# Optimization experiments

Hardware: AMD Instinct MI355X
Metric: run time of the kernel (lower is better)

Reference implementation:

```python
import jax, jax.numpy as jnp
import numpy as np
from jax import lax

B = 4096        # batch
D = 13          # state dim (13th component is constant context)
STEPS = 16      # output time points
SUBSTEPS = 2    # fixed dopri5 steps per output interval

# Dormand-Prince 5(4) tableau (5th-order solution row)
A21 = 1/5
A31, A32 = 3/40, 9/40
A41, A42, A43 = 44/45, -56/15, 32/9
A51, A52, A53, A54 = 19372/6561, -25360/2187, 64448/6561, -212/729
A61, A62, A63, A64, A65 = 9017/3168, -355/33, 46732/5247, 49/176, -5103/18656
B1, B3, B4, B5, B6 = 35/384, 500/1113, 125/192, -2187/6784, 11/84


def setup_inputs() -> dict:
    key = jax.random.key(0)
    ks = jax.random.split(key, 9)
    def lin(k, fin, fout):
        return jax.random.normal(k, (fin, fout), jnp.float32) / np.float32(np.sqrt(fin))
    return {
        "y0": jax.random.normal(ks[0], (B, D), jnp.float32),
        "t_span": jnp.arange(STEPS, dtype=jnp.float32) * 0.0625,  # total horizon 1.0
        "W1": lin(ks[1], 13, 256), "b1": jnp.zeros((256,), jnp.float32),
        "W2": lin(ks[2], 256, 256), "b2": jnp.zeros((256,), jnp.float32),
        "W3": lin(ks[3], 256, 128), "b3": jnp.zeros((128,), jnp.float32),
        "W4": lin(ks[4], 128, 12) * 0.1, "b4": jnp.zeros((12,), jnp.float32),
    }


def reference(y0, t_span, W1, b1, W2, b2, W3, b3, W4, b4):
    def f(y):  # learned derivative; 13th (context) component has zero derivative
        h = jax.nn.silu(y @ W1 + b1)
        h = jax.nn.silu(h @ W2 + b2)
        h = jax.nn.silu(h @ W3 + b3)
        d = h @ W4 + b4  # [B, 12]
        return jnp.concatenate([d, jnp.zeros_like(d[..., :1])], axis=-1)  # [B, 13]

    def rk_step(y, h):
        k1 = f(y)
        k2 = f(y + h * (A21 * k1))
        k3 = f(y + h * (A31 * k1 + A32 * k2))
        k4 = f(y + h * (A41 * k1 + A42 * k2 + A43 * k3))
        k5 = f(y + h * (A51 * k1 + A52 * k2 + A53 * k3 + A54 * k4))
        k6 = f(y + h * (A61 * k1 + A62 * k2 + A63 * k3 + A64 * k4 + A65 * k5))
        return y + h * (B1 * k1 + B3 * k3 + B4 * k4 + B5 * k5 + B6 * k6)

    # fixed step sizes: SUBSTEPS dopri5 steps per output interval
    hs = jnp.repeat(jnp.diff(t_span) / SUBSTEPS, SUBSTEPS)  # [(STEPS-1)*SUBSTEPS]

    def body(y, h):
        y = rk_step(y, h)
        return y, y

    _, ys = lax.scan(body, y0, hs)
    pred_y = jnp.concatenate([y0[None], ys[SUBSTEPS - 1::SUBSTEPS]], axis=0)  # [STEPS, B, 13]
    return pred_y
```

## Files before the change

kernel.cpp:

```cpp
#include <hip/hip_runtime.h>

typedef _Float16 f16;
typedef __attribute__((ext_vector_type(8))) _Float16 f16x8;
typedef __attribute__((ext_vector_type(4))) float f32x4;

#define MFMA16(a, b, c) __builtin_amdgcn_mfma_f32_16x16x32_f16((a), (b), (c), 0, 0, 0)

__device__ __forceinline__ float silu_f(float x) {
    return x * __builtin_amdgcn_rcpf(1.f + __expf(-x));
}

__device__ __forceinline__ void pack4(f16* dst, float x0, float x1, float x2, float x3) {
    union { f16 h[4]; uint2 u; } p;
    p.h[0] = (f16)x0; p.h[1] = (f16)x1; p.h[2] = (f16)x2; p.h[3] = (f16)x3;
    *(uint2*)dst = p.u;
}

__device__ __forceinline__ int pkf16(float a, float b) {
    typedef __attribute__((ext_vector_type(2))) __fp16 fp16x2;
    union { fp16x2 v; int i; } u;
    u.v = __builtin_amdgcn_cvt_pkrtz(a, b);
    return u.i;
}

__global__ __launch_bounds__(512, 2) void ode_main(
        const float* __restrict__ y0, const float* __restrict__ tspan,
        const float* __restrict__ W1, const float* __restrict__ b1,
        const float* __restrict__ W2, const float* __restrict__ b2,
        const float* __restrict__ W3, const float* __restrict__ b3,
        const float* __restrict__ W4, const float* __restrict__ b4,
        float* __restrict__ out) {

    __shared__ f16 h1[16 * 264];
    __shared__ f16 h2[16 * 264];
    __shared__ f16 h3[16 * 136];
    __shared__ float bias[656];
    __shared__ float tsh[16];

    const int tid = threadIdx.x;
    const int l = tid & 63, w = tid >> 6;
    const int g = l >> 4, col = l & 15;
    const int blk = blockIdx.x;
    const int bp0 = (32 * g + col) * 4;
    const int bp1 = bp0 + 64;

    f16x8 w1f[2], w2f[2][8], w3f[8], w4f[4];
#pragma unroll
    for (int a = 0; a < 2; ++a) {
        const int n = (2 * w + a) * 16 + col;
#pragma unroll
        for (int j = 0; j < 8; ++j) {
            const int k = g * 8 + j;
            w1f[a][j] = (k < 13) ? (f16)W1[k * 256 + n] : (f16)0.f;
        }
#pragma unroll
        for (int kt = 0; kt < 8; ++kt)
#pragma unroll
            for (int j = 0; j < 8; ++j)
                w2f[a][kt][j] = (f16)W2[(kt * 32 + g * 8 + j) * 256 + n];
    }
    {
        const int n3 = w * 16 + col;
#pragma unroll
        for (int kt = 0; kt < 8; ++kt)
#pragma unroll
            for (int j = 0; j < 8; ++j)
                w3f[kt][j] = (f16)W3[(kt * 32 + g * 8 + j) * 128 + n3];
    }
#pragma unroll
    for (int kt = 0; kt < 4; ++kt)
#pragma unroll
        for (int j = 0; j < 8; ++j)
            w4f[kt][j] = (col < 12) ? (f16)W4[(kt * 32 + g * 8 + j) * 12 + col] : (f16)0.f;

    for (int i = tid; i < 656; i += 512) {
        float v = 0.f;
        if (i < 256) v = b1[i];
        else if (i < 512) v = b2[i - 256];
        else if (i < 640) v = b3[i - 512];
        else if (i < 652) v = b4[i - 640];
        bias[i] = v;
    }
    if (tid < 16) tsh[tid] = tspan[tid];

    float yreg[4];
#pragma unroll
    for (int j = 0; j < 4; ++j) {
        const int c = 4 * g + j;
        yreg[j] = (c < 13) ? y0[(blk * 16 + col) * 13 + c] : 0.f;
    }
    if (w == 0) {
#pragma unroll
        for (int j = 0; j < 4; ++j) {
            const int c = 4 * g + j;
            if (c < 13) out[(size_t)(blk * 16 + col) * 13 + c] = yreg[j];
        }
    }
    __syncthreads();

    static constexpr float AT[5][5] = {
        {0.2f, 0.f, 0.f, 0.f, 0.f},
        {3.f/40.f, 9.f/40.f, 0.f, 0.f, 0.f},
        {44.f/45.f, -56.f/15.f, 32.f/9.f, 0.f, 0.f},
        {19372.f/6561.f, -25360.f/2187.f, 64448.f/6561.f, -212.f/729.f, 0.f},
        {9017.f/3168.f, -355.f/33.f, 46732.f/5247.f, 49.f/176.f, -5103.f/18656.f}
    };

    float kreg[6][4];
    f16x8 b0;
    {
        int h01 = pkf16(yreg[0], yreg[1]), h23 = pkf16(yreg[2], yreg[3]);
        int u0 = __builtin_amdgcn_ds_bpermute(bp0, h01);
        int u1 = __builtin_amdgcn_ds_bpermute(bp0, h23);
        int u2 = __builtin_amdgcn_ds_bpermute(bp1, h01);
        int u3 = __builtin_amdgcn_ds_bpermute(bp1, h23);
        if (g >= 2) { u0 = 0; u1 = 0; u2 = 0; u3 = 0; }
        union { int i[4]; f16x8 v; } u; u.i[0]=u0; u.i[1]=u1; u.i[2]=u2; u.i[3]=u3;
        b0 = u.v;
    }

    for (int step = 0; step < 30; ++step) {
        const float hstep = (tsh[(step >> 1) + 1] - tsh[step >> 1]) * 0.5f;
#pragma unroll
        for (int s = 0; s < 6; ++s) {
            f32x4 acc[2];
#pragma unroll
            for (int a = 0; a < 2; ++a) acc[a] = (f32x4){0.f, 0.f, 0.f, 0.f};
#pragma unroll
            for (int a = 0; a < 2; ++a) acc[a] = MFMA16(w1f[a], b0, acc[a]);
#pragma unroll
            for (int a = 0; a < 2; ++a) {
                const int nt = 2 * w + a;
                float4 bb = *(const float4*)&bias[nt * 16 + g * 4];
                pack4(&h1[col * 264 + nt * 16 + g * 4],
                      silu_f(acc[a][0] + bb.x), silu_f(acc[a][1] + bb.y),
                      silu_f(acc[a][2] + bb.z), silu_f(acc[a][3] + bb.w));
            }
            __syncthreads();
            f16x8 hf[8];
#pragma unroll
            for (int kt = 0; kt < 8; ++kt) hf[kt] = *(const f16x8*)&h1[col * 264 + kt * 32 + g * 8];
#pragma unroll
            for (int a = 0; a < 2; ++a) acc[a] = (f32x4){0.f, 0.f, 0.f, 0.f};
#pragma unroll
            for (int kt = 0; kt < 8; ++kt)
#pragma unroll
                for (int a = 0; a < 2; ++a) acc[a] = MFMA16(w2f[a][kt], hf[kt], acc[a]);
#pragma unroll
            for (int a = 0; a < 2; ++a) {
                const int nt = 2 * w + a;
                float4 bb = *(const float4*)&bias[256 + nt * 16 + g * 4];
                pack4(&h2[col * 264 + nt * 16 + g * 4],
                      silu_f(acc[a][0] + bb.x), silu_f(acc[a][1] + bb.y),
                      silu_f(acc[a][2] + bb.z), silu_f(acc[a][3] + bb.w));
            }
            __syncthreads();
#pragma unroll
            for (int kt = 0; kt < 8; ++kt) hf[kt] = *(const f16x8*)&h2[col * 264 + kt * 32 + g * 8];
            f32x4 a3 = (f32x4){0.f, 0.f, 0.f, 0.f};
#pragma unroll
            for (int kt = 0; kt < 8; ++kt) a3 = MFMA16(w3f[kt], hf[kt], a3);
            {
                float4 bb = *(const float4*)&bias[512 + w * 16 + g * 4];
                pack4(&h3[col * 136 + w * 16 + g * 4],
                      silu_f(a3[0] + bb.x), silu_f(a3[1] + bb.y),
                      silu_f(a3[2] + bb.z), silu_f(a3[3] + bb.w));
            }
            __syncthreads();
            f16x8 h3f[4];
#pragma unroll
            for (int kt = 0; kt < 4; ++kt) h3f[kt] = *(const f16x8*)&h3[col * 136 + kt * 32 + g * 8];
            f32x4 a4 = (f32x4){0.f, 0.f, 0.f, 0.f};
#pragma unroll
            for (int kt = 0; kt < 4; ++kt) a4 = MFMA16(w4f[kt], h3f[kt], a4);
            float4 bb4 = *(const float4*)&bias[640 + g * 4];
            kreg[s][0] = a4[0] + bb4.x; kreg[s][1] = a4[1] + bb4.y;
            kreg[s][2] = a4[2] + bb4.z; kreg[s][3] = a4[3] + bb4.w;
            float x[4];
            if (s < 5) {
#pragma unroll
                for (int j = 0; j < 4; ++j) {
                    float a2 = 0.f;
#pragma unroll
                    for (int i = 0; i <= s; ++i) a2 += AT[s][i] * kreg[i][j];
                    x[j] = yreg[j] + hstep * a2;
                }
            } else {
#pragma unroll
                for (int j = 0; j < 4; ++j) {
                    float a2 = (35.f/384.f) * kreg[0][j] + (500.f/1113.f) * kreg[2][j]
                             + (125.f/192.f) * kreg[3][j] + (-2187.f/6784.f) * kreg[4][j]
                             + (11.f/84.f) * kreg[5][j];
                    yreg[j] += hstep * a2;
                    x[j] = yreg[j];
                }
                if ((step & 1) && w == 0) {
                    const int slot = (step + 1) >> 1;
#pragma unroll
                    for (int j = 0; j < 4; ++j) {
                        const int c = 4 * g + j;
                        if (c < 13)
                            out[((size_t)slot * 4096 + blk * 16 + col) * 13 + c] = yreg[j];
                    }
                }
            }
            {
                int h01 = pkf16(x[0], x[1]), h23 = pkf16(x[2], x[3]);
                int u0 = __builtin_amdgcn_ds_bpermute(bp0, h01);
                int u1 = __builtin_amdgcn_ds_bpermute(bp0, h23);
                int u2 = __builtin_amdgcn_ds_bpermute(bp1, h01);
                int u3 = __builtin_amdgcn_ds_bpermute(bp1, h23);
                if (g >= 2) { u0 = 0; u1 = 0; u2 = 0; u3 = 0; }
                union { int i[4]; f16x8 v; } u; u.i[0]=u0; u.i[1]=u1; u.i[2]=u2; u.i[3]=u3;
                b0 = u.v;
            }
        }
    }
}

extern "C" void kernel_launch(void* const* d_in, const int* in_sizes, int n_in,
                              void* d_out, int out_size, void* d_ws, size_t ws_size,
                              hipStream_t stream) {
    (void)in_sizes; (void)n_in; (void)out_size; (void)d_ws; (void)ws_size;
    const float* y0 = (const float*)d_in[0];
    const float* ts = (const float*)d_in[1];
    const float* W1 = (const float*)d_in[2];
    const float* b1 = (const float*)d_in[3];
    const float* W2 = (const float*)d_in[4];
    const float* b2 = (const float*)d_in[5];
    const float* W3 = (const float*)d_in[6];
    const float* b3 = (const float*)d_in[7];
    const float* W4 = (const float*)d_in[8];
    const float* b4 = (const float*)d_in[9];
    float* out = (float*)d_out;

    hipLaunchKernelGGL(ode_main, dim3(256), dim3(512), 0, stream,
                       y0, ts, W1, b1, W2, b2, W3, b3, W4, b4, out);
}
```

Measured before the change: 361.9 us.

## Double wavefronts per block, move W3 to LDS, split MFMA accumulation chains

Each block now runs 1024 threads (16 waves), so every wave computes one 16-column tile of layers 1 and 2 instead of two. W3 fragments move from registers into a 64 KB LDS buffer and only 8 waves do layer 3. Stage derivatives are kept as packed fp16 to cut register pressure, and MFMA reductions are split into two independent accumulators to shorten dependency chains. The goals are more latency hiding per CU and lower VGPR use. The costs are extra LDS traffic for W3, idle waves during layers 3 and 4, fp16 rounding of the RK stage values, and barrier cost across 16 waves.

```diff
diff --git a/kernel.cpp b/kernel.cpp
--- a/kernel.cpp
+++ b/kernel.cpp
@@ -8,12 +8,6 @@
 
 __device__ __forceinline__ float silu_f(float x) {
     return x * __builtin_amdgcn_rcpf(1.f + __expf(-x));
-}
-
-__device__ __forceinline__ void pack4(f16* dst, float x0, float x1, float x2, float x3) {
-    union { f16 h[4]; uint2 u; } p;
-    p.h[0] = (f16)x0; p.h[1] = (f16)x1; p.h[2] = (f16)x2; p.h[3] = (f16)x3;
-    *(uint2*)dst = p.u;
 }
 
 __device__ __forceinline__ int pkf16(float a, float b) {
@@ -23,7 +17,17 @@
     return u.i;
 }
 
-__global__ __launch_bounds__(512, 2) void ode_main(
+__device__ __forceinline__ void pack4(f16* dst, float a, float b, float c, float d) {
+    uint2 u; u.x = (unsigned)pkf16(a, b); u.y = (unsigned)pkf16(c, d);
+    *(uint2*)dst = u;
+}
+
+__device__ __forceinline__ float upk(int u, int hi) {
+    union { __fp16 h[2]; int i; } x; x.i = u;
+    return (float)x.h[hi];
+}
+
+__global__ __launch_bounds__(1024, 4) void ode_main(
         const float* __restrict__ y0, const float* __restrict__ tspan,
         const float* __restrict__ W1, const float* __restrict__ b1,
         const float* __restrict__ W2, const float* __restrict__ b2,
@@ -31,6 +35,7 @@
         const float* __restrict__ W4, const float* __restrict__ b4,
         float* __restrict__ out) {
 
+    __shared__ f16 w3l[64 * 512];
     __shared__ f16 h1[16 * 264];
     __shared__ f16 h2[16 * 264];
     __shared__ f16 h3[16 * 136];
@@ -44,28 +49,19 @@
     const int bp0 = (32 * g + col) * 4;
     const int bp1 = bp0 + 64;
 
-    f16x8 w1f[2], w2f[2][8], w3f[8], w4f[4];
-#pragma unroll
-    for (int a = 0; a < 2; ++a) {
-        const int n = (2 * w + a) * 16 + col;
+    f16x8 w1f, w2f[8], w4f[4];
+    {
+        const int n = w * 16 + col;
 #pragma unroll
         for (int j = 0; j < 8; ++j) {
             const int k = g * 8 + j;
-            w1f[a][j] = (k < 13) ? (f16)W1[k * 256 + n] : (f16)0.f;
+            w1f[j] = (k < 13) ? (f16)W1[k * 256 + n] : (f16)0.f;
         }
 #pragma unroll
         for (int kt = 0; kt < 8; ++kt)
 #pragma unroll
             for (int j = 0; j < 8; ++j)
-                w2f[a][kt][j] = (f16)W2[(kt * 32 + g * 8 + j) * 256 + n];
-    }
-    {
-        const int n3 = w * 16 + col;
-#pragma unroll
-        for (int kt = 0; kt < 8; ++kt)
-#pragma unroll
-            for (int j = 0; j < 8; ++j)
-                w3f[kt][j] = (f16)W3[(kt * 32 + g * 8 + j) * 128 + n3];
+                w2f[kt][j] = (f16)W2[(kt * 32 + g * 8 + j) * 256 + n];
     }
 #pragma unroll
     for (int kt = 0; kt < 4; ++kt)
@@ -73,7 +69,17 @@
         for (int j = 0; j < 8; ++j)
             w4f[kt][j] = (col < 12) ? (f16)W4[(kt * 32 + g * 8 + j) * 12 + col] : (f16)0.f;
 
-    for (int i = tid; i < 656; i += 512) {
+#pragma unroll
+    for (int q = 0; q < 4; ++q) {
+        const int f = w * 4 + q, nt = f >> 3, kt = f & 7;
+        f16x8 tv;
+#pragma unroll
+        for (int j = 0; j < 8; ++j)
+            tv[j] = (f16)W3[(kt * 32 + g * 8 + j) * 128 + nt * 16 + col];
+        *(f16x8*)&w3l[f * 512 + l * 8] = tv;
+    }
+
+    for (int i = tid; i < 656; i += 1024) {
         float v = 0.f;
         if (i < 256) v = b1[i];
         else if (i < 512) v = b2[i - 256];
@@ -106,7 +112,7 @@
         {9017.f/3168.f, -355.f/33.f, 46732.f/5247.f, 49.f/176.f, -5103.f/18656.f}
     };
 
-    float kreg[6][4];
+    int kpk[6][2];
     f16x8 b0;
     {
         int h01 = pkf16(yreg[0], yreg[1]), h23 = pkf16(yreg[2], yreg[3]);
@@ -123,84 +129,91 @@
         const float hstep = (tsh[(step >> 1) + 1] - tsh[step >> 1]) * 0.5f;
 #pragma unroll
         for (int s = 0; s < 6; ++s) {
-            f32x4 acc[2];
-#pragma unroll
-            for (int a = 0; a < 2; ++a) acc[a] = (f32x4){0.f, 0.f, 0.f, 0.f};
-#pragma unroll
-            for (int a = 0; a < 2; ++a) acc[a] = MFMA16(w1f[a], b0, acc[a]);
-#pragma unroll
-            for (int a = 0; a < 2; ++a) {
-                const int nt = 2 * w + a;
-                float4 bb = *(const float4*)&bias[nt * 16 + g * 4];
-                pack4(&h1[col * 264 + nt * 16 + g * 4],
-                      silu_f(acc[a][0] + bb.x), silu_f(acc[a][1] + bb.y),
-                      silu_f(acc[a][2] + bb.z), silu_f(acc[a][3] + bb.w));
+            {
+                f32x4 acc = MFMA16(w1f, b0, ((f32x4){0.f,0.f,0.f,0.f}));
+                float4 bb = *(const float4*)&bias[w * 16 + g * 4];
+                pack4(&h1[col * 264 + w * 16 + g * 4],
+                      silu_f(acc[0] + bb.x), silu_f(acc[1] + bb.y),
+                      silu_f(acc[2] + bb.z), silu_f(acc[3] + bb.w));
             }
             __syncthreads();
-            f16x8 hf[8];
-#pragma unroll
-            for (int kt = 0; kt < 8; ++kt) hf[kt] = *(const f16x8*)&h1[col * 264 + kt * 32 + g * 8];
-#pragma unroll
-            for (int a = 0; a < 2; ++a) acc[a] = (f32x4){0.f, 0.f, 0.f, 0.f};
-#pragma unroll
-            for (int kt = 0; kt < 8; ++kt)
-#pragma unroll
-                for (int a = 0; a < 2; ++a) acc[a] = MFMA16(w2f[a][kt], hf[kt], acc[a]);
-#pragma unroll
-            for (int a = 0; a < 2; ++a) {
-                const int nt = 2 * w + a;
-                float4 bb = *(const float4*)&bias[256 + nt * 16 + g * 4];
-                pack4(&h2[col * 264 + nt * 16 + g * 4],
-                      silu_f(acc[a][0] + bb.x), silu_f(acc[a][1] + bb.y),
-                      silu_f(acc[a][2] + bb.z), silu_f(acc[a][3] + bb.w));
+            {
+                f32x4 aL = (f32x4){0.f,0.f,0.f,0.f}, aH = aL;
+#pragma unroll
+                for (int kt = 0; kt < 4; ++kt) {
+                    f16x8 hL = *(const f16x8*)&h1[col * 264 + kt * 32 + g * 8];
+                    f16x8 hH = *(const f16x8*)&h1[col * 264 + (kt + 4) * 32 + g * 8];
+                    aL = MFMA16(w2f[kt], hL, aL);
+                    aH = MFMA16(w2f[kt + 4], hH, aH);
+                }
+                f32x4 acc = aL + aH;
+                float4 bb = *(const float4*)&bias[256 + w * 16 + g * 4];
+                pack4(&h2[col * 264 + w * 16 + g * 4],
+                      silu_f(acc[0] + bb.x), silu_f(acc[1] + bb.y),
+                      silu_f(acc[2] + bb.z), silu_f(acc[3] + bb.w));
             }
             __syncthreads();
-#pragma unroll
-            for (int kt = 0; kt < 8; ++kt) hf[kt] = *(const f16x8*)&h2[col * 264 + kt * 32 + g * 8];
-            f32x4 a3 = (f32x4){0.f, 0.f, 0.f, 0.f};
-#pragma unroll
-            for (int kt = 0; kt < 8; ++kt) a3 = MFMA16(w3f[kt], hf[kt], a3);
-            {
+            if (w < 8) {
+                f32x4 aL = (f32x4){0.f,0.f,0.f,0.f}, aH = aL;
+#pragma unroll
+                for (int kt = 0; kt < 4; ++kt) {
+                    f16x8 wL = *(const f16x8*)&w3l[(w * 8 + kt) * 512 + l * 8];
+                    f16x8 hL = *(const f16x8*)&h2[col * 264 + kt * 32 + g * 8];
+                    aL = MFMA16(wL, hL, aL);
+                    f16x8 wH = *(const f16x8*)&w3l[(w * 8 + kt + 4) * 512 + l * 8];
+                    f16x8 hH = *(const f16x8*)&h2[col * 264 + (kt + 4) * 32 + g * 8];
+                    aH = MFMA16(wH, hH, aH);
+                }
+                f32x4 acc = aL + aH;
                 float4 bb = *(const float4*)&bias[512 + w * 16 + g * 4];
                 pack4(&h3[col * 136 + w * 16 + g * 4],
-                      silu_f(a3[0] + bb.x), silu_f(a3[1] + bb.y),
-                      silu_f(a3[2] + bb.z), silu_f(a3[3] + bb.w));
+                      silu_f(acc[0] + bb.x), silu_f(acc[1] + bb.y),
+                      silu_f(acc[2] + bb.z), silu_f(acc[3] + bb.w));
             }
             __syncthreads();
-            f16x8 h3f[4];
-#pragma unroll
-            for (int kt = 0; kt < 4; ++kt) h3f[kt] = *(const f16x8*)&h3[col * 136 + kt * 32 + g * 8];
-            f32x4 a4 = (f32x4){0.f, 0.f, 0.f, 0.f};
-#pragma unroll
-            for (int kt = 0; kt < 4; ++kt) a4 = MFMA16(w4f[kt], h3f[kt], a4);
-            float4 bb4 = *(const float4*)&bias[640 + g * 4];
-            kreg[s][0] = a4[0] + bb4.x; kreg[s][1] = a4[1] + bb4.y;
-            kreg[s][2] = a4[2] + bb4.z; kreg[s][3] = a4[3] + bb4.w;
             float x[4];
-            if (s < 5) {
-#pragma unroll
-                for (int j = 0; j < 4; ++j) {
-                    float a2 = 0.f;
-#pragma unroll
-                    for (int i = 0; i <= s; ++i) a2 += AT[s][i] * kreg[i][j];
-                    x[j] = yreg[j] + hstep * a2;
-                }
-            } else {
-#pragma unroll
-                for (int j = 0; j < 4; ++j) {
-                    float a2 = (35.f/384.f) * kreg[0][j] + (500.f/1113.f) * kreg[2][j]
-                             + (125.f/192.f) * kreg[3][j] + (-2187.f/6784.f) * kreg[4][j]
-                             + (11.f/84.f) * kreg[5][j];
-                    yreg[j] += hstep * a2;
-                    x[j] = yreg[j];
-                }
-                if ((step & 1) && w == 0) {
-                    const int slot = (step + 1) >> 1;
+            {
+                f32x4 aL = (f32x4){0.f,0.f,0.f,0.f}, aH = aL;
+#pragma unroll
+                for (int kt = 0; kt < 2; ++kt) {
+                    f16x8 hL = *(const f16x8*)&h3[col * 136 + kt * 32 + g * 8];
+                    aL = MFMA16(w4f[kt], hL, aL);
+                    f16x8 hH = *(const f16x8*)&h3[col * 136 + (kt + 2) * 32 + g * 8];
+                    aH = MFMA16(w4f[kt + 2], hH, aH);
+                }
+                f32x4 a4 = aL + aH;
+                float4 bb4 = *(const float4*)&bias[640 + g * 4];
+                float kc[4] = {a4[0] + bb4.x, a4[1] + bb4.y, a4[2] + bb4.z, a4[3] + bb4.w};
+                kpk[s][0] = pkf16(kc[0], kc[1]);
+                kpk[s][1] = pkf16(kc[2], kc[3]);
+                if (s < 5) {
 #pragma unroll
                     for (int j = 0; j < 4; ++j) {
-                        const int c = 4 * g + j;
-                        if (c < 13)
-                            out[((size_t)slot * 4096 + blk * 16 + col) * 13 + c] = yreg[j];
+                        float a2 = AT[s][s] * kc[j];
+#pragma unroll
+                        for (int i = 0; i < 5; ++i)
+                            if (i < s) a2 += AT[s][i] * upk(kpk[i][j >> 1], j & 1);
+                        x[j] = yreg[j] + hstep * a2;
+                    }
+                } else {
+#pragma unroll
+                    for (int j = 0; j < 4; ++j) {
+                        float a2 = (35.f/384.f)   * upk(kpk[0][j >> 1], j & 1)
+                                 + (500.f/1113.f) * upk(kpk[2][j >> 1], j & 1)
+                                 + (125.f/192.f)  * upk(kpk[3][j >> 1], j & 1)
+                                 + (-2187.f/6784.f) * upk(kpk[4][j >> 1], j & 1)
+                                 + (11.f/84.f)    * kc[j];
+                        yreg[j] += hstep * a2;
+                        x[j] = yreg[j];
+                    }
+                    if ((step & 1) && w == 0) {
+                        const int slot = (step + 1) >> 1;
+#pragma unroll
+                        for (int j = 0; j < 4; ++j) {
+                            const int c = 4 * g + j;
+                            if (c < 13)
+                                out[((size_t)slot * 4096 + blk * 16 + col) * 13 + c] = yreg[j];
+                        }
                     }
                 }
             }
@@ -234,6 +247,6 @@
     const float* b4 = (const float*)d_in[9];
     float* out = (float*)d_out;
 
-    hipLaunchKernelGGL(ode_main, dim3(256), dim3(512), 0, stream,
+    hipLaunchKernelGGL(ode_main, dim3(256), dim3(1024), 0, stream,
                        y0, ts, W1, b1, W2, b2, W3, b3, W4, b4, out);
 }
```

Measured after the change: 434.3 us. 1.2x slower.
